# Kernel optimization log

Measured on AMD Instinct MI355X. Metric: run time of the kernel, lower is better.

The kernel has to match this reference:

```python
import jax, jax.numpy as jnp
import numpy as np

S, L, K = 4, 256, 32          # num_states, seq length, neighbors
ORIG_H, EMB_H, EXV, RANK = 128, 256, 384, 16


def _integrate(x, Wq, Wk, seq_idx, emb_idx, hidden, rank):
    """AttentionIntegrator.forward: QK^T softmax -> double mean -> softmax -> weighted pool of raw x."""
    x = jnp.moveaxis(x, (seq_idx, emb_idx), (-2, -1))
    orig_shape = x.shape
    Ls = orig_shape[-2]
    xf = x.reshape(-1, Ls, hidden)               # (B, Ls, hidden)
    B = xf.shape[0]
    q = (xf @ Wq.T).reshape(B, Ls, rank, hidden)  # head_dim == hidden
    k = (xf @ Wk.T).reshape(B, Ls, rank, hidden)
    scale = 1.0 / jnp.sqrt(jnp.asarray(hidden, xf.dtype))
    scores = jnp.einsum('blhd,bmhd->bhlm', q, k) * scale
    attn = jax.nn.softmax(scores, axis=-1)        # (B, rank, Ls, Ls)
    w = jax.nn.softmax(attn.mean(axis=(1, 2)), axis=-1)  # (B, Ls)
    pooled = jnp.einsum('bl,bld->bd', w, xf)      # (B, hidden)
    return (pooled.reshape(*orig_shape[:-2], hidden),
            w.reshape(*orig_shape[:-2], Ls))


def setup_inputs() -> dict:
    key = jax.random.key(0)
    ks = jax.random.split(key, 12)
    sc = lambda fan_in: 1.0 / np.sqrt(fan_in)
    return {
        'h_V':    jax.random.normal(ks[0], (S, L, ORIG_H), jnp.float32),
        'h_EXV':  jax.random.normal(ks[1], (S, L, K, EXV), jnp.float32),
        'W_hV':   jax.random.normal(ks[2], (EMB_H, ORIG_H), jnp.float32) * sc(ORIG_H),
        'b_hV':   jnp.zeros((EMB_H,), jnp.float32),
        'Wq_hv':  jax.random.normal(ks[3], (RANK * EMB_H, EMB_H), jnp.float32) * sc(EMB_H),
        'Wk_hv':  jax.random.normal(ks[4], (RANK * EMB_H, EMB_H), jnp.float32) * sc(EMB_H),
        'Wq_ce':  jax.random.normal(ks[5], (RANK * EXV, EXV), jnp.float32) * sc(EXV),
        'Wk_ce':  jax.random.normal(ks[6], (RANK * EXV, EXV), jnp.float32) * sc(EXV),
        'W_ce':   jax.random.normal(ks[7], (EMB_H, EXV), jnp.float32) * sc(EXV),
        'b_ce':   jnp.zeros((EMB_H,), jnp.float32),
        'Wq_sce': jax.random.normal(ks[8], (RANK * EMB_H, EMB_H), jnp.float32) * sc(EMB_H),
        'Wk_sce': jax.random.normal(ks[9], (RANK * EMB_H, EMB_H), jnp.float32) * sc(EMB_H),
    }


def reference(h_V, h_EXV, W_hV, b_hV, Wq_hv, Wk_hv, Wq_ce, Wk_ce, W_ce, b_ce, Wq_sce, Wk_sce):
    # diffmodel.get_weights
    hv = h_V @ W_hV.T + b_hV                                  # (S, L, EMB_H)
    h_V_int, h_V_w = _integrate(hv, Wq_hv, Wk_hv, 0, 2, EMB_H, RANK)   # pool over states
    # chemical environment: pool over k neighbors per (state, position)
    ce, _local_w = _integrate(h_EXV, Wq_ce, Wk_ce, 2, 3, EXV, RANK)    # (S, L, EXV)
    ce = ce @ W_ce.T + b_ce                                   # (S, L, EMB_H)
    ce_int, ce_w = _integrate(ce, Wq_sce, Wk_sce, 0, 2, EMB_H, RANK)   # pool over states
    return (h_V_int[None], h_V_w[None], ce_int[None], ce_w[None])
```

## Files before the change

### kernel.cpp

```cpp
#include <hip/hip_runtime.h>

typedef _Float16 f16;
typedef _Float16 f16x8 __attribute__((ext_vector_type(8)));
typedef _Float16 f16x4 __attribute__((ext_vector_type(4)));
typedef float f32x4 __attribute__((ext_vector_type(4)));

#define MFMA16(a, b, c) __builtin_amdgcn_mfma_f32_16x16x32_f16(a, b, c, 0, 0, 0)
#define MFMA16K16(a, b, c) __builtin_amdgcn_mfma_f32_16x16x16f16(a, b, c, 0, 0, 0)

__global__ __launch_bounds__(256) void k_mt3(const float* __restrict__ Wq_hv,
                                             const float* __restrict__ Wk_hv,
                                             f16* __restrict__ mt_hv,
                                             const float* __restrict__ Wq_ce,
                                             const float* __restrict__ Wk_ce,
                                             f16* __restrict__ mt_ce,
                                             const float* __restrict__ Wq_sce,
                                             const float* __restrict__ Wk_sce,
                                             f16* __restrict__ mt_sce) {
    const int y = blockIdx.y;
    const float *Wq, *Wk;
    f16* MT;
    int H, ty;
    if (y < 16)      { Wq = Wq_hv;  Wk = Wk_hv;  MT = mt_hv;  H = 256; ty = y; }
    else if (y < 52) { Wq = Wq_ce;  Wk = Wk_ce;  MT = mt_ce;  H = 384; ty = y - 16; }
    else             { Wq = Wq_sce; Wk = Wk_sce; MT = mt_sce; H = 256; ty = y - 52; }

    const int h = blockIdx.x;
    const int ntile = H >> 6;
    const int nkk = H >> 5;
    const int frow = (ty / ntile) * 64;
    const int ecol = (ty % ntile) * 64;
    const int t = threadIdx.x;
    const int lane = t & 63;
    const int w = t >> 6;
    const int wr = w >> 1, wc = w & 1;

    __shared__ __align__(16) f16 As[64][40];
    __shared__ __align__(16) f16 Ks[64][40];

    f32x4 acc[2][2] = {};
    const int d = t >> 3;
    const int e8 = (t & 7) * 8;

    for (int kk = 0; kk < nkk; ++kk) {
        const float* gq = Wq + (size_t)(h * H + kk * 32 + d) * H + ecol + e8;
        const float* gk = Wk + (size_t)(h * H + kk * 32 + d) * H + frow + e8;
        float q[8], k[8];
#pragma unroll
        for (int i = 0; i < 8; ++i) { q[i] = gq[i]; k[i] = gk[i]; }
        __syncthreads();
#pragma unroll
        for (int i = 0; i < 8; ++i) { As[e8 + i][d] = (f16)q[i]; Ks[e8 + i][d] = (f16)k[i]; }
        __syncthreads();
        f16x8 a[2], b[2];
#pragma unroll
        for (int rt = 0; rt < 2; ++rt)
            a[rt] = *(const f16x8*)&Ks[wr * 32 + rt * 16 + (lane & 15)][(lane >> 4) * 8];
#pragma unroll
        for (int nt = 0; nt < 2; ++nt)
            b[nt] = *(const f16x8*)&As[wc * 32 + nt * 16 + (lane & 15)][(lane >> 4) * 8];
#pragma unroll
        for (int rt = 0; rt < 2; ++rt)
#pragma unroll
            for (int nt = 0; nt < 2; ++nt)
                acc[rt][nt] = MFMA16(a[rt], b[nt], acc[rt][nt]);
    }
#pragma unroll
    for (int rt = 0; rt < 2; ++rt)
#pragma unroll
        for (int nt = 0; nt < 2; ++nt)
#pragma unroll
            for (int j = 0; j < 4; ++j) {
                int f = frow + wr * 32 + rt * 16 + (lane >> 4) * 4 + j;
                int e = ecol + wc * 32 + nt * 16 + (lane & 15);
                MT[(((size_t)h * nkk + (e >> 5)) * H + f) * 32 + (e & 31)] = (f16)acc[rt][nt][j];
            }
}

__global__ __launch_bounds__(256) void k_lin(const float* __restrict__ in,
                                             const float* __restrict__ W,
                                             const float* __restrict__ bias,
                                             float* __restrict__ out, int K) {
    const int t = threadIdx.x;
    const int r0 = blockIdx.x * 4;
    __shared__ float ins[4][384];
    __shared__ float Ws[256][33];
#pragma unroll
    for (int r = 0; r < 4; ++r)
        for (int off = t; off < K; off += 256)
            ins[r][off] = in[(size_t)(r0 + r) * K + off];
    float acc[4] = {};
    for (int d0 = 0; d0 < K; d0 += 32) {
        __syncthreads();
        for (int i = t; i < 256 * 32; i += 256) {
            int j = i >> 5, dd = i & 31;
            Ws[j][dd] = W[(size_t)j * K + d0 + dd];
        }
        __syncthreads();
#pragma unroll 8
        for (int dd = 0; dd < 32; ++dd) {
            float wv = Ws[t][dd];
#pragma unroll
            for (int r = 0; r < 4; ++r) acc[r] += wv * ins[r][d0 + dd];
        }
    }
    float bv = bias[t];
#pragma unroll
    for (int r = 0; r < 4; ++r) out[(size_t)(r0 + r) * 256 + t] = acc[r] + bv;
}

__global__ __launch_bounds__(256) void k_small_int(const float* __restrict__ X,
                                                   const f16* __restrict__ MT,
                                                   float* __restrict__ wpart) {
    const int t = threadIdx.x;
    const int lane = t & 63;
    const int w = t >> 6;
    const int g = lane >> 4;
    const int l15 = lane & 15;
    const int pos0 = blockIdx.x * 8;
    const int h = blockIdx.y;

    __shared__ __align__(16) f16 Xs[32][264];
    __shared__ __align__(16) f16 Ts[32][264];

    {
        int row = t >> 3, d0 = (t & 7) * 32;
        int s = row & 3, p = row >> 2;
        const float* gx = X + (size_t)(s * 256 + pos0 + p) * 256 + d0;
#pragma unroll
        for (int i = 0; i < 32; i += 8) {
            float4 v0 = *(const float4*)(gx + i);
            float4 v1 = *(const float4*)(gx + i + 4);
            f16x8 o;
            o[0] = (f16)v0.x; o[1] = (f16)v0.y; o[2] = (f16)v0.z; o[3] = (f16)v0.w;
            o[4] = (f16)v1.x; o[5] = (f16)v1.y; o[6] = (f16)v1.z; o[7] = (f16)v1.w;
            *(f16x8*)&Xs[row][d0 + i] = o;
        }
    }
    __syncthreads();

    const f16* mh = MT + (size_t)h * 8 * 256 * 32;
    const int fb = w * 64 + l15;
    f32x4 acc[2][4] = {};
    f16x8 bq[4], bn[4];
#pragma unroll
    for (int nt = 0; nt < 4; ++nt)
        bq[nt] = *(const f16x8*)(mh + (size_t)(fb + nt * 16) * 32 + g * 8);
#pragma unroll
    for (int kk = 0; kk < 8; ++kk) {
        if (kk < 7) {
#pragma unroll
            for (int nt = 0; nt < 4; ++nt)
                bn[nt] = *(const f16x8*)(mh + ((size_t)(kk + 1) * 256 + fb + nt * 16) * 32 + g * 8);
        }
        f16x8 a[2];
#pragma unroll
        for (int mt = 0; mt < 2; ++mt)
            a[mt] = *(const f16x8*)&Xs[mt * 16 + l15][kk * 32 + g * 8];
#pragma unroll
        for (int mt = 0; mt < 2; ++mt)
#pragma unroll
            for (int nt = 0; nt < 4; ++nt)
                acc[mt][nt] = MFMA16(a[mt], bq[nt], acc[mt][nt]);
#pragma unroll
        for (int nt = 0; nt < 4; ++nt) bq[nt] = bn[nt];
    }
#pragma unroll
    for (int mt = 0; mt < 2; ++mt)
#pragma unroll
        for (int nt = 0; nt < 4; ++nt)
#pragma unroll
            for (int j = 0; j < 4; ++j)
                Ts[mt * 16 + g * 4 + j][w * 64 + nt * 16 + l15] = (f16)acc[mt][nt][j];
    __syncthreads();

    if (w < 2) {
        f32x4 sacc = {};
#pragma unroll
        for (int ks = 0; ks < 8; ++ks) {
            f16x8 a = *(const f16x8*)&Ts[w * 16 + l15][ks * 32 + g * 8];
            f16x8 b = *(const f16x8*)&Xs[w * 16 + l15][ks * 32 + g * 8];
            sacc = MFMA16(a, b, sacc);
        }
        if ((l15 >> 2) == g) {
            const float scale = 1.0f / 16.0f;
            float add = 0.f;
#pragma unroll
            for (int j = 0; j < 4; ++j) {
                float v = sacc[j] * scale;
                float m = v;
                m = fmaxf(m, __shfl_xor(m, 1));
                m = fmaxf(m, __shfl_xor(m, 2));
                float e = expf(v - m);
                float s2 = e;
                s2 += __shfl_xor(s2, 1);
                s2 += __shfl_xor(s2, 2);
                add += e / s2;
            }
            int pg = pos0 + w * 4 + g;
            wpart[((size_t)h * 256 + pg) * 4 + (l15 & 3)] = add;
        }
    }
}

__global__ __launch_bounds__(256) void k_small_fin(const float* __restrict__ wpart,
                                                   const float* __restrict__ X,
                                                   float* __restrict__ out_int,
                                                   float* __restrict__ out_w) {
    const int pos = blockIdx.x, t = threadIdx.x;
    __shared__ float red[64];
    __shared__ float ws[4];
    if (t < 64) red[t] = wpart[((size_t)(t >> 2) * 256 + pos) * 4 + (t & 3)];
    __syncthreads();
    if (t == 0) {
        float v[4];
#pragma unroll
        for (int s = 0; s < 4; ++s) {
            float x = 0.f;
            for (int hh = 0; hh < 16; ++hh) x += red[hh * 4 + s];
            v[s] = x * (1.0f / 64.0f);
        }
        float m = fmaxf(fmaxf(v[0], v[1]), fmaxf(v[2], v[3]));
        float sum = 0.f;
#pragma unroll
        for (int s = 0; s < 4; ++s) { v[s] = expf(v[s] - m); sum += v[s]; }
#pragma unroll
        for (int s = 0; s < 4; ++s) ws[s] = v[s] / sum;
    }
    __syncthreads();
    if (t < 4) out_w[pos * 4 + t] = ws[t];
    float v = 0.f;
#pragma unroll
    for (int s = 0; s < 4; ++s) v += ws[s] * X[(size_t)(s * 256 + pos) * 256 + t];
    out_int[(size_t)pos * 256 + t] = v;
}

__global__ __launch_bounds__(512) void k_ce_int(const float* __restrict__ Xg32,
                                                const f16* __restrict__ MT,
                                                float* __restrict__ acc_out) {
    const int t = threadIdx.x;
    const int lane = t & 63;
    const int w = t >> 6;
    const int g = lane >> 4;
    const int l15 = lane & 15;
    const int bg = blockIdx.x;

    extern __shared__ __align__(16) char smem[];

    {
        const float* xg = Xg32 + (size_t)bg * 64 * 384;
#pragma unroll
        for (int p = 0; p < 6; ++p) {
            int idx = p * 512 + t;
            int row = idx / 48, s = idx - row * 48;
            int c = s ^ (row & 7);
            const float* src = xg + row * 384 + c * 8;
            float4 v0 = *(const float4*)src;
            float4 v1 = *(const float4*)(src + 4);
            f16x8 o;
            o[0] = (f16)v0.x; o[1] = (f16)v0.y; o[2] = (f16)v0.z; o[3] = (f16)v0.w;
            o[4] = (f16)v1.x; o[5] = (f16)v1.y; o[6] = (f16)v1.z; o[7] = (f16)v1.w;
            *(f16x8*)(smem + idx * 16) = o;
        }
    }
    __syncthreads();

    const float scale = 0.051031036307982884f;

    for (int h2 = 0; h2 < 2; ++h2) {
        const int h = h2 * 8 + w;
        const f16* mh = MT + (size_t)h * 12 * 12288;

        f32x4 S2[2][2][2] = {};

        f16x8 A[2][2];
#pragma unroll
        for (int ft = 0; ft < 2; ++ft)
            A[0][ft] = *(const f16x8*)(mh + (size_t)(0 * 32 + ft * 16 + l15) * 32 + g * 8);

        for (int c = 0; c < 12; ++c) {
            f32x4 acc[2][4] = {};
#pragma unroll
            for (int kk = 0; kk < 12; ++kk) {
                const int step = c * 12 + kk;
                {
                    int ns = step + 1;
                    int nc = ns / 12, nk = ns - nc * 12;
                    if (nc > 11) { nc = 11; nk = 11; }
#pragma unroll
                    for (int ft = 0; ft < 2; ++ft)
                        A[(step + 1) & 1][ft] =
                            *(const f16x8*)(mh + (size_t)nk * 12288 +
                                            (size_t)(nc * 32 + ft * 16 + l15) * 32 + g * 8);
                }
                f16x8 xb[4];
#pragma unroll
                for (int mt = 0; mt < 4; ++mt) {
                    int row = mt * 16 + l15;
                    int ch = kk * 4 + g;
                    xb[mt] = *(const f16x8*)(smem + row * 768 + ((ch ^ (row & 7)) << 4));
                }
                __builtin_amdgcn_s_setprio(1);
#pragma unroll
                for (int ft = 0; ft < 2; ++ft)
#pragma unroll
                    for (int mt = 0; mt < 4; ++mt)
                        acc[ft][mt] = MFMA16(A[step & 1][ft], xb[mt], acc[ft][mt]);
                __builtin_amdgcn_s_setprio(0);
            }

            f16x4 bf[2][4];
#pragma unroll
            for (int ft = 0; ft < 2; ++ft)
#pragma unroll
                for (int mt = 0; mt < 4; ++mt) {
                    f32x4 v = acc[ft][mt];
                    f16x4 o;
                    o[0] = (f16)v[0]; o[1] = (f16)v[1]; o[2] = (f16)v[2]; o[3] = (f16)v[3];
                    bf[ft][mt] = o;
                }

#pragma unroll
            for (int b = 0; b < 2; ++b)
#pragma unroll
                for (int ks = 0; ks < 2; ++ks)
#pragma unroll
                    for (int it = 0; it < 2; ++it) {
                        int row = b * 32 + it * 16 + l15;
                        int ch = c * 4 + ks * 2 + (g >> 1);
                        f16x4 av = *(const f16x4*)(smem + row * 768 +
                                                   ((ch ^ (row & 7)) << 4) + 8 * (g & 1));
#pragma unroll
                        for (int lt = 0; lt < 2; ++lt)
                            S2[b][it][lt] = MFMA16K16(av, bf[ks][2 * b + lt], S2[b][it][lt]);
                    }
        }

#pragma unroll
        for (int b = 0; b < 2; ++b)
#pragma unroll
            for (int it = 0; it < 2; ++it) {
                f32x4 sum0 = S2[b][it][0];
                f32x4 sum1 = S2[b][it][1];
                float cs0 = 0.f, cs1 = 0.f;
#pragma unroll
                for (int j = 0; j < 4; ++j) {
                    float v0 = sum0[j] * scale, v1 = sum1[j] * scale;
                    float m = fmaxf(v0, v1);
                    m = fmaxf(m, __shfl_xor(m, 1));
                    m = fmaxf(m, __shfl_xor(m, 2));
                    m = fmaxf(m, __shfl_xor(m, 4));
                    m = fmaxf(m, __shfl_xor(m, 8));
                    float e0 = __expf(v0 - m), e1 = __expf(v1 - m);
                    float s = e0 + e1;
                    s += __shfl_xor(s, 1);
                    s += __shfl_xor(s, 2);
                    s += __shfl_xor(s, 4);
                    s += __shfl_xor(s, 8);
                    float inv = 1.f / s;
                    cs0 += e0 * inv;
                    cs1 += e1 * inv;
                }
                cs0 += __shfl_xor(cs0, 16); cs0 += __shfl_xor(cs0, 32);
                cs1 += __shfl_xor(cs1, 16); cs1 += __shfl_xor(cs1, 32);
                if (lane < 16) {
                    float* o = acc_out + (((size_t)h * 1024 + bg * 2 + b) * 2 + it) * 32;
                    o[l15] = cs0;
                    o[16 + l15] = cs1;
                }
            }
    }
}

__global__ __launch_bounds__(256) void k_ce_pool(const float* __restrict__ accp,
                                                 const float* __restrict__ exv,
                                                 float* __restrict__ pooled) {
    const int b = blockIdx.x;
    const int t = threadIdx.x;
    __shared__ float ww[32];
    if (t < 32) {
        float s = 0.f;
#pragma unroll
        for (int h = 0; h < 16; ++h) {
            s += accp[(((size_t)h * 1024 + b) * 2 + 0) * 32 + t];
            s += accp[(((size_t)h * 1024 + b) * 2 + 1) * 32 + t];
        }
        s *= (1.0f / 512.0f);
        float m = s;
        m = fmaxf(m, __shfl_xor(m, 1));
        m = fmaxf(m, __shfl_xor(m, 2));
        m = fmaxf(m, __shfl_xor(m, 4));
        m = fmaxf(m, __shfl_xor(m, 8));
        m = fmaxf(m, __shfl_xor(m, 16));
        float e = __expf(s - m);
        float sum = e;
        sum += __shfl_xor(sum, 1);
        sum += __shfl_xor(sum, 2);
        sum += __shfl_xor(sum, 4);
        sum += __shfl_xor(sum, 8);
        sum += __shfl_xor(sum, 16);
        ww[t] = e / sum;
    }
    __syncthreads();
    for (int d = t; d < 384; d += 256) {
        float v = 0.f;
#pragma unroll
        for (int m = 0; m < 32; ++m) v += ww[m] * exv[((size_t)b * 32 + m) * 384 + d];
        pooled[(size_t)b * 384 + d] = v;
    }
}

extern "C" void kernel_launch(void* const* d_in, const int* in_sizes, int n_in,
                              void* d_out, int out_size, void* d_ws, size_t ws_size,
                              hipStream_t stream) {
    const float* h_V    = (const float*)d_in[0];
    const float* h_EXV  = (const float*)d_in[1];
    const float* W_hV   = (const float*)d_in[2];
    const float* b_hV   = (const float*)d_in[3];
    const float* Wq_hv  = (const float*)d_in[4];
    const float* Wk_hv  = (const float*)d_in[5];
    const float* Wq_ce  = (const float*)d_in[6];
    const float* Wk_ce  = (const float*)d_in[7];
    const float* W_ce   = (const float*)d_in[8];
    const float* b_ce   = (const float*)d_in[9];
    const float* Wq_sce = (const float*)d_in[10];
    const float* Wk_sce = (const float*)d_in[11];
    float* out = (float*)d_out;

    char* ws = (char*)d_ws;
    f16*   mt_hv  = (f16*)(ws + 0);
    f16*   mt_sce = (f16*)(ws + 2097152);
    f16*   mt_ce  = (f16*)(ws + 4194304);
    float* hv     = (float*)(ws + 8912896);
    float* ce     = (float*)(ws + 9961472);
    float* accp   = (float*)(ws + 11010048);
    float* pooled = (float*)(ws + 15204352);
    float* wpart  = accp;

    k_mt3<<<dim3(16, 68), 256, 0, stream>>>(Wq_hv, Wk_hv, mt_hv,
                                            Wq_ce, Wk_ce, mt_ce,
                                            Wq_sce, Wk_sce, mt_sce);
    k_lin<<<256, 256, 0, stream>>>(h_V, W_hV, b_hV, hv, 128);
    k_small_int<<<dim3(32, 16), 256, 0, stream>>>(hv, mt_hv, wpart);
    k_small_fin<<<256, 256, 0, stream>>>(wpart, hv, out + 0, out + 65536);
    k_ce_int<<<dim3(512), 512, 49152, stream>>>(h_EXV, mt_ce, accp);
    k_ce_pool<<<1024, 256, 0, stream>>>(accp, h_EXV, pooled);
    k_lin<<<256, 256, 0, stream>>>(pooled, W_ce, b_ce, ce, 384);
    k_small_int<<<dim3(32, 16), 256, 0, stream>>>(ce, mt_sce, wpart);
    k_small_fin<<<256, 256, 0, stream>>>(wpart, ce, out + 66560, out + 132096);
}
```

Before: 304.3 us.

## Merge independent launches into horizontally fused kernels to cut launch count

Combines the weight-transform kernel with the h_V linear layer, the big ce attention kernel with the small hv attention kernel, and the ce pooling with the hv final reduction, dispatching by block index. This drops three launches and lets the independent hv branch run alongside the ce work instead of serially. The small-branch paths use larger dynamic shared memory and 512-thread blocks where only half the threads work, which may lower occupancy for those blocks. wpart moves to its own workspace region so it no longer aliases accp.

Measured after the change: 286.8 us. 1.06x faster.

```diff
diff --git a/kernel.cpp b/kernel.cpp
--- a/kernel.cpp
+++ b/kernel.cpp
@@ -8,73 +8,109 @@
 #define MFMA16(a, b, c) __builtin_amdgcn_mfma_f32_16x16x32_f16(a, b, c, 0, 0, 0)
 #define MFMA16K16(a, b, c) __builtin_amdgcn_mfma_f32_16x16x16f16(a, b, c, 0, 0, 0)
 
-__global__ __launch_bounds__(256) void k_mt3(const float* __restrict__ Wq_hv,
-                                             const float* __restrict__ Wk_hv,
-                                             f16* __restrict__ mt_hv,
-                                             const float* __restrict__ Wq_ce,
-                                             const float* __restrict__ Wk_ce,
-                                             f16* __restrict__ mt_ce,
-                                             const float* __restrict__ Wq_sce,
-                                             const float* __restrict__ Wk_sce,
-                                             f16* __restrict__ mt_sce) {
-    const int y = blockIdx.y;
-    const float *Wq, *Wk;
-    f16* MT;
-    int H, ty;
-    if (y < 16)      { Wq = Wq_hv;  Wk = Wk_hv;  MT = mt_hv;  H = 256; ty = y; }
-    else if (y < 52) { Wq = Wq_ce;  Wk = Wk_ce;  MT = mt_ce;  H = 384; ty = y - 16; }
-    else             { Wq = Wq_sce; Wk = Wk_sce; MT = mt_sce; H = 256; ty = y - 52; }
-
-    const int h = blockIdx.x;
-    const int ntile = H >> 6;
-    const int nkk = H >> 5;
-    const int frow = (ty / ntile) * 64;
-    const int ecol = (ty % ntile) * 64;
+__global__ __launch_bounds__(256) void k_front(const float* __restrict__ Wq_hv,
+                                               const float* __restrict__ Wk_hv,
+                                               f16* __restrict__ mt_hv,
+                                               const float* __restrict__ Wq_ce,
+                                               const float* __restrict__ Wk_ce,
+                                               f16* __restrict__ mt_ce,
+                                               const float* __restrict__ Wq_sce,
+                                               const float* __restrict__ Wk_sce,
+                                               f16* __restrict__ mt_sce,
+                                               const float* __restrict__ h_V,
+                                               const float* __restrict__ W_hV,
+                                               const float* __restrict__ b_hV,
+                                               float* __restrict__ hv) {
+    extern __shared__ __align__(16) char smem[];
+    const int bid = blockIdx.x;
     const int t = threadIdx.x;
-    const int lane = t & 63;
-    const int w = t >> 6;
-    const int wr = w >> 1, wc = w & 1;
-
-    __shared__ __align__(16) f16 As[64][40];
-    __shared__ __align__(16) f16 Ks[64][40];
-
-    f32x4 acc[2][2] = {};
-    const int d = t >> 3;
-    const int e8 = (t & 7) * 8;
-
-    for (int kk = 0; kk < nkk; ++kk) {
-        const float* gq = Wq + (size_t)(h * H + kk * 32 + d) * H + ecol + e8;
-        const float* gk = Wk + (size_t)(h * H + kk * 32 + d) * H + frow + e8;
-        float q[8], k[8];
-#pragma unroll
-        for (int i = 0; i < 8; ++i) { q[i] = gq[i]; k[i] = gk[i]; }
-        __syncthreads();
-#pragma unroll
-        for (int i = 0; i < 8; ++i) { As[e8 + i][d] = (f16)q[i]; Ks[e8 + i][d] = (f16)k[i]; }
-        __syncthreads();
-        f16x8 a[2], b[2];
+
+    if (bid < 1088) {
+        const int h = bid & 15;
+        const int y = bid >> 4;
+        const float *Wq, *Wk;
+        f16* MT;
+        int H, ty;
+        if (y < 16)      { Wq = Wq_hv;  Wk = Wk_hv;  MT = mt_hv;  H = 256; ty = y; }
+        else if (y < 52) { Wq = Wq_ce;  Wk = Wk_ce;  MT = mt_ce;  H = 384; ty = y - 16; }
+        else             { Wq = Wq_sce; Wk = Wk_sce; MT = mt_sce; H = 256; ty = y - 52; }
+
+        const int ntile = H >> 6;
+        const int nkk = H >> 5;
+        const int frow = (ty / ntile) * 64;
+        const int ecol = (ty % ntile) * 64;
+        const int lane = t & 63;
+        const int w = t >> 6;
+        const int wr = w >> 1, wc = w & 1;
+
+        f16(*As)[40] = (f16(*)[40])smem;
+        f16(*Ks)[40] = (f16(*)[40])(smem + 5120);
+
+        f32x4 acc[2][2] = {};
+        const int d = t >> 3;
+        const int e8 = (t & 7) * 8;
+
+        for (int kk = 0; kk < nkk; ++kk) {
+            const float* gq = Wq + (size_t)(h * H + kk * 32 + d) * H + ecol + e8;
+            const float* gk = Wk + (size_t)(h * H + kk * 32 + d) * H + frow + e8;
+            float q[8], k[8];
+#pragma unroll
+            for (int i = 0; i < 8; ++i) { q[i] = gq[i]; k[i] = gk[i]; }
+            __syncthreads();
+#pragma unroll
+            for (int i = 0; i < 8; ++i) { As[e8 + i][d] = (f16)q[i]; Ks[e8 + i][d] = (f16)k[i]; }
+            __syncthreads();
+            f16x8 a[2], b[2];
+#pragma unroll
+            for (int rt = 0; rt < 2; ++rt)
+                a[rt] = *(const f16x8*)&Ks[wr * 32 + rt * 16 + (lane & 15)][(lane >> 4) * 8];
+#pragma unroll
+            for (int nt = 0; nt < 2; ++nt)
+                b[nt] = *(const f16x8*)&As[wc * 32 + nt * 16 + (lane & 15)][(lane >> 4) * 8];
+#pragma unroll
+            for (int rt = 0; rt < 2; ++rt)
+#pragma unroll
+                for (int nt = 0; nt < 2; ++nt)
+                    acc[rt][nt] = MFMA16(a[rt], b[nt], acc[rt][nt]);
+        }
 #pragma unroll
         for (int rt = 0; rt < 2; ++rt)
-            a[rt] = *(const f16x8*)&Ks[wr * 32 + rt * 16 + (lane & 15)][(lane >> 4) * 8];
-#pragma unroll
-        for (int nt = 0; nt < 2; ++nt)
-            b[nt] = *(const f16x8*)&As[wc * 32 + nt * 16 + (lane & 15)][(lane >> 4) * 8];
-#pragma unroll
-        for (int rt = 0; rt < 2; ++rt)
 #pragma unroll
             for (int nt = 0; nt < 2; ++nt)
-                acc[rt][nt] = MFMA16(a[rt], b[nt], acc[rt][nt]);
-    }
-#pragma unroll
-    for (int rt = 0; rt < 2; ++rt)
-#pragma unroll
-        for (int nt = 0; nt < 2; ++nt)
-#pragma unroll
-            for (int j = 0; j < 4; ++j) {
-                int f = frow + wr * 32 + rt * 16 + (lane >> 4) * 4 + j;
-                int e = ecol + wc * 32 + nt * 16 + (lane & 15);
-                MT[(((size_t)h * nkk + (e >> 5)) * H + f) * 32 + (e & 31)] = (f16)acc[rt][nt][j];
-            }
+#pragma unroll
+                for (int j = 0; j < 4; ++j) {
+                    int f = frow + wr * 32 + rt * 16 + (lane >> 4) * 4 + j;
+                    int e = ecol + wc * 32 + nt * 16 + (lane & 15);
+                    MT[(((size_t)h * nkk + (e >> 5)) * H + f) * 32 + (e & 31)] = (f16)acc[rt][nt][j];
+                }
+    } else {
+        const int r0 = (bid - 1088) * 4;
+        const int K = 128;
+        float(*ins)[384] = (float(*)[384])smem;
+        float(*Ws)[33] = (float(*)[33])(smem + 6144);
+#pragma unroll
+        for (int r = 0; r < 4; ++r)
+            for (int off = t; off < K; off += 256)
+                ins[r][off] = h_V[(size_t)(r0 + r) * K + off];
+        float acc[4] = {};
+        for (int d0 = 0; d0 < K; d0 += 32) {
+            __syncthreads();
+            for (int i = t; i < 256 * 32; i += 256) {
+                int j = i >> 5, dd = i & 31;
+                Ws[j][dd] = W_hV[(size_t)j * K + d0 + dd];
+            }
+            __syncthreads();
+#pragma unroll 8
+            for (int dd = 0; dd < 32; ++dd) {
+                float wv = Ws[t][dd];
+#pragma unroll
+                for (int r = 0; r < 4; ++r) acc[r] += wv * ins[r][d0 + dd];
+            }
+        }
+        float bv = b_hV[t];
+#pragma unroll
+        for (int r = 0; r < 4; ++r) hv[(size_t)(r0 + r) * 256 + t] = acc[r] + bv;
+    }
 }
 
 __global__ __launch_bounds__(256) void k_lin(const float* __restrict__ in,
@@ -235,178 +271,303 @@
     out_int[(size_t)pos * 256 + t] = v;
 }
 
-__global__ __launch_bounds__(512) void k_ce_int(const float* __restrict__ Xg32,
-                                                const f16* __restrict__ MT,
-                                                float* __restrict__ acc_out) {
+__global__ __launch_bounds__(512) void k_mid(const float* __restrict__ Xg32,
+                                             const f16* __restrict__ MTce,
+                                             float* __restrict__ acc_out,
+                                             const float* __restrict__ hv,
+                                             const f16* __restrict__ MThv,
+                                             float* __restrict__ wpart) {
+    extern __shared__ __align__(16) char smem[];
     const int t = threadIdx.x;
     const int lane = t & 63;
     const int w = t >> 6;
     const int g = lane >> 4;
     const int l15 = lane & 15;
-    const int bg = blockIdx.x;
-
-    extern __shared__ __align__(16) char smem[];
-
-    {
-        const float* xg = Xg32 + (size_t)bg * 64 * 384;
-#pragma unroll
-        for (int p = 0; p < 6; ++p) {
-            int idx = p * 512 + t;
-            int row = idx / 48, s = idx - row * 48;
-            int c = s ^ (row & 7);
-            const float* src = xg + row * 384 + c * 8;
-            float4 v0 = *(const float4*)src;
-            float4 v1 = *(const float4*)(src + 4);
-            f16x8 o;
-            o[0] = (f16)v0.x; o[1] = (f16)v0.y; o[2] = (f16)v0.z; o[3] = (f16)v0.w;
-            o[4] = (f16)v1.x; o[5] = (f16)v1.y; o[6] = (f16)v1.z; o[7] = (f16)v1.w;
-            *(f16x8*)(smem + idx * 16) = o;
-        }
-    }
-    __syncthreads();
-
-    const float scale = 0.051031036307982884f;
-
-    for (int h2 = 0; h2 < 2; ++h2) {
-        const int h = h2 * 8 + w;
-        const f16* mh = MT + (size_t)h * 12 * 12288;
-
-        f32x4 S2[2][2][2] = {};
-
-        f16x8 A[2][2];
-#pragma unroll
-        for (int ft = 0; ft < 2; ++ft)
-            A[0][ft] = *(const f16x8*)(mh + (size_t)(0 * 32 + ft * 16 + l15) * 32 + g * 8);
-
-        for (int c = 0; c < 12; ++c) {
+
+    if (blockIdx.x < 512) {
+        const int bg = blockIdx.x;
+        {
+            const float* xg = Xg32 + (size_t)bg * 64 * 384;
+#pragma unroll
+            for (int p = 0; p < 6; ++p) {
+                int idx = p * 512 + t;
+                int row = idx / 48, s = idx - row * 48;
+                int c = s ^ (row & 7);
+                const float* src = xg + row * 384 + c * 8;
+                float4 v0 = *(const float4*)src;
+                float4 v1 = *(const float4*)(src + 4);
+                f16x8 o;
+                o[0] = (f16)v0.x; o[1] = (f16)v0.y; o[2] = (f16)v0.z; o[3] = (f16)v0.w;
+                o[4] = (f16)v1.x; o[5] = (f16)v1.y; o[6] = (f16)v1.z; o[7] = (f16)v1.w;
+                *(f16x8*)(smem + idx * 16) = o;
+            }
+        }
+        __syncthreads();
+
+        const float scale = 0.051031036307982884f;
+
+        for (int h2 = 0; h2 < 2; ++h2) {
+            const int h = h2 * 8 + w;
+            const f16* mh = MTce + (size_t)h * 12 * 12288;
+
+            f32x4 S2[2][2][2] = {};
+            f16x8 A[2][2];
+#pragma unroll
+            for (int ft = 0; ft < 2; ++ft)
+                A[0][ft] = *(const f16x8*)(mh + (size_t)(ft * 16 + l15) * 32 + g * 8);
+
+            for (int c = 0; c < 12; ++c) {
+                f32x4 acc[2][4] = {};
+#pragma unroll
+                for (int kk = 0; kk < 12; ++kk) {
+                    const int step = c * 12 + kk;
+                    {
+                        int ns = step + 1;
+                        int nc = ns / 12, nk = ns - nc * 12;
+                        if (nc > 11) { nc = 11; nk = 11; }
+#pragma unroll
+                        for (int ft = 0; ft < 2; ++ft)
+                            A[(step + 1) & 1][ft] =
+                                *(const f16x8*)(mh + (size_t)nk * 12288 +
+                                                (size_t)(nc * 32 + ft * 16 + l15) * 32 + g * 8);
+                    }
+                    f16x8 xb[4];
+#pragma unroll
+                    for (int mt = 0; mt < 4; ++mt) {
+                        int row = mt * 16 + l15;
+                        int ch = kk * 4 + g;
+                        xb[mt] = *(const f16x8*)(smem + row * 768 + ((ch ^ (row & 7)) << 4));
+                    }
+                    __builtin_amdgcn_s_setprio(1);
+#pragma unroll
+                    for (int ft = 0; ft < 2; ++ft)
+#pragma unroll
+                        for (int mt = 0; mt < 4; ++mt)
+                            acc[ft][mt] = MFMA16(A[step & 1][ft], xb[mt], acc[ft][mt]);
+                    __builtin_amdgcn_s_setprio(0);
+                }
+
+                f16x4 bf[2][4];
+#pragma unroll
+                for (int ft = 0; ft < 2; ++ft)
+#pragma unroll
+                    for (int mt = 0; mt < 4; ++mt) {
+                        f32x4 v = acc[ft][mt];
+                        f16x4 o;
+                        o[0] = (f16)v[0]; o[1] = (f16)v[1]; o[2] = (f16)v[2]; o[3] = (f16)v[3];
+                        bf[ft][mt] = o;
+                    }
+
+#pragma unroll
+                for (int b = 0; b < 2; ++b)
+#pragma unroll
+                    for (int ks = 0; ks < 2; ++ks)
+#pragma unroll
+                        for (int it = 0; it < 2; ++it) {
+                            int row = b * 32 + it * 16 + l15;
+                            int ch = c * 4 + ks * 2 + (g >> 1);
+                            f16x4 av = *(const f16x4*)(smem + row * 768 +
+                                                       ((ch ^ (row & 7)) << 4) + 8 * (g & 1));
+#pragma unroll
+                            for (int lt = 0; lt < 2; ++lt)
+                                S2[b][it][lt] = MFMA16K16(av, bf[ks][2 * b + lt], S2[b][it][lt]);
+                        }
+            }
+
+#pragma unroll
+            for (int b = 0; b < 2; ++b)
+#pragma unroll
+                for (int it = 0; it < 2; ++it) {
+                    f32x4 sum0 = S2[b][it][0];
+                    f32x4 sum1 = S2[b][it][1];
+                    float cs0 = 0.f, cs1 = 0.f;
+#pragma unroll
+                    for (int j = 0; j < 4; ++j) {
+                        float v0 = sum0[j] * scale, v1 = sum1[j] * scale;
+                        float m = fmaxf(v0, v1);
+                        m = fmaxf(m, __shfl_xor(m, 1));
+                        m = fmaxf(m, __shfl_xor(m, 2));
+                        m = fmaxf(m, __shfl_xor(m, 4));
+                        m = fmaxf(m, __shfl_xor(m, 8));
+                        float e0 = __expf(v0 - m), e1 = __expf(v1 - m);
+                        float s = e0 + e1;
+                        s += __shfl_xor(s, 1);
+                        s += __shfl_xor(s, 2);
+                        s += __shfl_xor(s, 4);
+                        s += __shfl_xor(s, 8);
+                        float inv = 1.f / s;
+                        cs0 += e0 * inv;
+                        cs1 += e1 * inv;
+                    }
+                    cs0 += __shfl_xor(cs0, 16); cs0 += __shfl_xor(cs0, 32);
+                    cs1 += __shfl_xor(cs1, 16); cs1 += __shfl_xor(cs1, 32);
+                    if (lane < 16) {
+                        float* o = acc_out + (((size_t)h * 1024 + bg * 2 + b) * 2 + it) * 32;
+                        o[l15] = cs0;
+                        o[16 + l15] = cs1;
+                    }
+                }
+        }
+    } else {
+        const int bid2 = blockIdx.x - 512;
+        const int pos0 = (bid2 & 31) * 8;
+        const int h = bid2 >> 5;
+
+        f16(*Xs)[264] = (f16(*)[264])smem;
+        f16(*Ts)[264] = (f16(*)[264])(smem + 16896);
+
+        if (t < 256) {
+            int row = t >> 3, d0 = (t & 7) * 32;
+            int s = row & 3, p = row >> 2;
+            const float* gx = hv + (size_t)(s * 256 + pos0 + p) * 256 + d0;
+#pragma unroll
+            for (int i = 0; i < 32; i += 8) {
+                float4 v0 = *(const float4*)(gx + i);
+                float4 v1 = *(const float4*)(gx + i + 4);
+                f16x8 o;
+                o[0] = (f16)v0.x; o[1] = (f16)v0.y; o[2] = (f16)v0.z; o[3] = (f16)v0.w;
+                o[4] = (f16)v1.x; o[5] = (f16)v1.y; o[6] = (f16)v1.z; o[7] = (f16)v1.w;
+                *(f16x8*)&Xs[row][d0 + i] = o;
+            }
+        }
+        __syncthreads();
+
+        if (t < 256) {
+            const f16* mh = MThv + (size_t)h * 8 * 256 * 32;
+            const int fb = w * 64 + l15;
             f32x4 acc[2][4] = {};
-#pragma unroll
-            for (int kk = 0; kk < 12; ++kk) {
-                const int step = c * 12 + kk;
-                {
-                    int ns = step + 1;
-                    int nc = ns / 12, nk = ns - nc * 12;
-                    if (nc > 11) { nc = 11; nk = 11; }
-#pragma unroll
-                    for (int ft = 0; ft < 2; ++ft)
-                        A[(step + 1) & 1][ft] =
-                            *(const f16x8*)(mh + (size_t)nk * 12288 +
-                                            (size_t)(nc * 32 + ft * 16 + l15) * 32 + g * 8);
+            f16x8 bq[4], bn[4];
+#pragma unroll
+            for (int nt = 0; nt < 4; ++nt)
+                bq[nt] = *(const f16x8*)(mh + (size_t)(fb + nt * 16) * 32 + g * 8);
+#pragma unroll
+            for (int kk = 0; kk < 8; ++kk) {
+                if (kk < 7) {
+#pragma unroll
+                    for (int nt = 0; nt < 4; ++nt)
+                        bn[nt] = *(const f16x8*)(mh + ((size_t)(kk + 1) * 256 + fb + nt * 16) * 32 + g * 8);
                 }
-                f16x8 xb[4];
-#pragma unroll
-                for (int mt = 0; mt < 4; ++mt) {
-                    int row = mt * 16 + l15;
-                    int ch = kk * 4 + g;
-                    xb[mt] = *(const f16x8*)(smem + row * 768 + ((ch ^ (row & 7)) << 4));
-                }
-                __builtin_amdgcn_s_setprio(1);
-#pragma unroll
-                for (int ft = 0; ft < 2; ++ft)
-#pragma unroll
-                    for (int mt = 0; mt < 4; ++mt)
-                        acc[ft][mt] = MFMA16(A[step & 1][ft], xb[mt], acc[ft][mt]);
-                __builtin_amdgcn_s_setprio(0);
-            }
-
-            f16x4 bf[2][4];
-#pragma unroll
-            for (int ft = 0; ft < 2; ++ft)
-#pragma unroll
-                for (int mt = 0; mt < 4; ++mt) {
-                    f32x4 v = acc[ft][mt];
-                    f16x4 o;
-                    o[0] = (f16)v[0]; o[1] = (f16)v[1]; o[2] = (f16)v[2]; o[3] = (f16)v[3];
-                    bf[ft][mt] = o;
-                }
-
-#pragma unroll
-            for (int b = 0; b < 2; ++b)
-#pragma unroll
-                for (int ks = 0; ks < 2; ++ks)
-#pragma unroll
-                    for (int it = 0; it < 2; ++it) {
-                        int row = b * 32 + it * 16 + l15;
-                        int ch = c * 4 + ks * 2 + (g >> 1);
-                        f16x4 av = *(const f16x4*)(smem + row * 768 +
-                                                   ((ch ^ (row & 7)) << 4) + 8 * (g & 1));
-#pragma unroll
-                        for (int lt = 0; lt < 2; ++lt)
-                            S2[b][it][lt] = MFMA16K16(av, bf[ks][2 * b + lt], S2[b][it][lt]);
-                    }
-        }
-
-#pragma unroll
-        for (int b = 0; b < 2; ++b)
-#pragma unroll
-            for (int it = 0; it < 2; ++it) {
-                f32x4 sum0 = S2[b][it][0];
-                f32x4 sum1 = S2[b][it][1];
-                float cs0 = 0.f, cs1 = 0.f;
+                f16x8 a[2];
+#pragma unroll
+                for (int mt = 0; mt < 2; ++mt)
+                    a[mt] = *(const f16x8*)&Xs[mt * 16 + l15][kk * 32 + g * 8];
+#pragma unroll
+                for (int mt = 0; mt < 2; ++mt)
+#pragma unroll
+                    for (int nt = 0; nt < 4; ++nt)
+                        acc[mt][nt] = MFMA16(a[mt], bq[nt], acc[mt][nt]);
+#pragma unroll
+                for (int nt = 0; nt < 4; ++nt) bq[nt] = bn[nt];
+            }
+#pragma unroll
+            for (int mt = 0; mt < 2; ++mt)
+#pragma unroll
+                for (int nt = 0; nt < 4; ++nt)
+#pragma unroll
+                    for (int j = 0; j < 4; ++j)
+                        Ts[mt * 16 + g * 4 + j][w * 64 + nt * 16 + l15] = (f16)acc[mt][nt][j];
+        }
+        __syncthreads();
+
+        if (t < 128) {
+            f32x4 sacc = {};
+#pragma unroll
+            for (int ks = 0; ks < 8; ++ks) {
+                f16x8 a = *(const f16x8*)&Ts[w * 16 + l15][ks * 32 + g * 8];
+                f16x8 b = *(const f16x8*)&Xs[w * 16 + l15][ks * 32 + g * 8];
+                sacc = MFMA16(a, b, sacc);
+            }
+            if ((l15 >> 2) == g) {
+                const float scale = 1.0f / 16.0f;
+                float add = 0.f;
 #pragma unroll
                 for (int j = 0; j < 4; ++j) {
-                    float v0 = sum0[j] * scale, v1 = sum1[j] * scale;
-                    float m = fmaxf(v0, v1);
+                    float v = sacc[j] * scale;
+                    float m = v;
                     m = fmaxf(m, __shfl_xor(m, 1));
                     m = fmaxf(m, __shfl_xor(m, 2));
-                    m = fmaxf(m, __shfl_xor(m, 4));
-                    m = fmaxf(m, __shfl_xor(m, 8));
-                    float e0 = __expf(v0 - m), e1 = __expf(v1 - m);
-                    float s = e0 + e1;
-                    s += __shfl_xor(s, 1);
-                    s += __shfl_xor(s, 2);
-                    s += __shfl_xor(s, 4);
-                    s += __shfl_xor(s, 8);
-                    float inv = 1.f / s;
-                    cs0 += e0 * inv;
-                    cs1 += e1 * inv;
+                    float e = expf(v - m);
+                    float s2 = e;
+                    s2 += __shfl_xor(s2, 1);
+                    s2 += __shfl_xor(s2, 2);
+                    add += e / s2;
                 }
-                cs0 += __shfl_xor(cs0, 16); cs0 += __shfl_xor(cs0, 32);
-                cs1 += __shfl_xor(cs1, 16); cs1 += __shfl_xor(cs1, 32);
-                if (lane < 16) {
-                    float* o = acc_out + (((size_t)h * 1024 + bg * 2 + b) * 2 + it) * 32;
-                    o[l15] = cs0;
-                    o[16 + l15] = cs1;
-                }
-            }
+                int pg = pos0 + w * 4 + g;
+                wpart[((size_t)h * 256 + pg) * 4 + (l15 & 3)] = add;
+            }
+        }
     }
 }
 
-__global__ __launch_bounds__(256) void k_ce_pool(const float* __restrict__ accp,
-                                                 const float* __restrict__ exv,
-                                                 float* __restrict__ pooled) {
-    const int b = blockIdx.x;
+__global__ __launch_bounds__(256) void k_back(const float* __restrict__ accp,
+                                              const float* __restrict__ exv,
+                                              float* __restrict__ pooled,
+                                              const float* __restrict__ wpart,
+                                              const float* __restrict__ hv,
+                                              float* __restrict__ out_int,
+                                              float* __restrict__ out_w) {
     const int t = threadIdx.x;
     __shared__ float ww[32];
-    if (t < 32) {
-        float s = 0.f;
-#pragma unroll
-        for (int h = 0; h < 16; ++h) {
-            s += accp[(((size_t)h * 1024 + b) * 2 + 0) * 32 + t];
-            s += accp[(((size_t)h * 1024 + b) * 2 + 1) * 32 + t];
-        }
-        s *= (1.0f / 512.0f);
-        float m = s;
-        m = fmaxf(m, __shfl_xor(m, 1));
-        m = fmaxf(m, __shfl_xor(m, 2));
-        m = fmaxf(m, __shfl_xor(m, 4));
-        m = fmaxf(m, __shfl_xor(m, 8));
-        m = fmaxf(m, __shfl_xor(m, 16));
-        float e = __expf(s - m);
-        float sum = e;
-        sum += __shfl_xor(sum, 1);
-        sum += __shfl_xor(sum, 2);
-        sum += __shfl_xor(sum, 4);
-        sum += __shfl_xor(sum, 8);
-        sum += __shfl_xor(sum, 16);
-        ww[t] = e / sum;
-    }
-    __syncthreads();
-    for (int d = t; d < 384; d += 256) {
+    __shared__ float red[64];
+    __shared__ float ws[4];
+
+    if (blockIdx.x < 1024) {
+        const int b = blockIdx.x;
+        if (t < 32) {
+            float s = 0.f;
+#pragma unroll
+            for (int h = 0; h < 16; ++h) {
+                s += accp[(((size_t)h * 1024 + b) * 2 + 0) * 32 + t];
+                s += accp[(((size_t)h * 1024 + b) * 2 + 1) * 32 + t];
+            }
+            s *= (1.0f / 512.0f);
+            float m = s;
+            m = fmaxf(m, __shfl_xor(m, 1));
+            m = fmaxf(m, __shfl_xor(m, 2));
+            m = fmaxf(m, __shfl_xor(m, 4));
+            m = fmaxf(m, __shfl_xor(m, 8));
+            m = fmaxf(m, __shfl_xor(m, 16));
+            float e = __expf(s - m);
+            float sum = e;
+            sum += __shfl_xor(sum, 1);
+            sum += __shfl_xor(sum, 2);
+            sum += __shfl_xor(sum, 4);
+            sum += __shfl_xor(sum, 8);
+            sum += __shfl_xor(sum, 16);
+            ww[t] = e / sum;
+        }
+        __syncthreads();
+        for (int d = t; d < 384; d += 256) {
+            float v = 0.f;
+#pragma unroll
+            for (int m = 0; m < 32; ++m) v += ww[m] * exv[((size_t)b * 32 + m) * 384 + d];
+            pooled[(size_t)b * 384 + d] = v;
+        }
+    } else {
+        const int pos = blockIdx.x - 1024;
+        if (t < 64) red[t] = wpart[((size_t)(t >> 2) * 256 + pos) * 4 + (t & 3)];
+        __syncthreads();
+        if (t == 0) {
+            float v[4];
+#pragma unroll
+            for (int s = 0; s < 4; ++s) {
+                float x = 0.f;
+                for (int hh = 0; hh < 16; ++hh) x += red[hh * 4 + s];
+                v[s] = x * (1.0f / 64.0f);
+            }
+            float m = fmaxf(fmaxf(v[0], v[1]), fmaxf(v[2], v[3]));
+            float sum = 0.f;
+#pragma unroll
+            for (int s = 0; s < 4; ++s) { v[s] = expf(v[s] - m); sum += v[s]; }
+#pragma unroll
+            for (int s = 0; s < 4; ++s) ws[s] = v[s] / sum;
+        }
+        __syncthreads();
+        if (t < 4) out_w[pos * 4 + t] = ws[t];
         float v = 0.f;
 #pragma unroll
-        for (int m = 0; m < 32; ++m) v += ww[m] * exv[((size_t)b * 32 + m) * 384 + d];
-        pooled[(size_t)b * 384 + d] = v;
+        for (int s = 0; s < 4; ++s) v += ws[s] * hv[(size_t)(s * 256 + pos) * 256 + t];
+        out_int[(size_t)pos * 256 + t] = v;
     }
 }
 
@@ -435,16 +596,15 @@
     float* ce     = (float*)(ws + 9961472);
     float* accp   = (float*)(ws + 11010048);
     float* pooled = (float*)(ws + 15204352);
-    float* wpart  = accp;
-
-    k_mt3<<<dim3(16, 68), 256, 0, stream>>>(Wq_hv, Wk_hv, mt_hv,
-                                            Wq_ce, Wk_ce, mt_ce,
-                                            Wq_sce, Wk_sce, mt_sce);
-    k_lin<<<256, 256, 0, stream>>>(h_V, W_hV, b_hV, hv, 128);
-    k_small_int<<<dim3(32, 16), 256, 0, stream>>>(hv, mt_hv, wpart);
-    k_small_fin<<<256, 256, 0, stream>>>(wpart, hv, out + 0, out + 65536);
-    k_ce_int<<<dim3(512), 512, 49152, stream>>>(h_EXV, mt_ce, accp);
-    k_ce_pool<<<1024, 256, 0, stream>>>(accp, h_EXV, pooled);
+    float* wpart  = (float*)(ws + 16777216);
+
+    k_front<<<1344, 256, 39936, stream>>>(Wq_hv, Wk_hv, mt_hv,
+                                          Wq_ce, Wk_ce, mt_ce,
+                                          Wq_sce, Wk_sce, mt_sce,
+                                          h_V, W_hV, b_hV, hv);
+    k_mid<<<1024, 512, 49152, stream>>>(h_EXV, mt_ce, accp, hv, mt_hv, wpart);
+    k_back<<<1280, 256, 0, stream>>>(accp, h_EXV, pooled, wpart, hv,
+                                     out + 0, out + 65536);
     k_lin<<<256, 256, 0, stream>>>(pooled, W_ce, b_ce, ce, 384);
     k_small_int<<<dim3(32, 16), 256, 0, stream>>>(ce, mt_sce, wpart);
     k_small_fin<<<256, 256, 0, stream>>>(wpart, ce, out + 66560, out + 132096);
```
